# Kernel optimization log

Hardware: AMD Instinct MI355X
Metric: run time of the kernel (lower is better)

Reference implementation:

```python
import jax, jax.numpy as jnp
import numpy as np

EMB = 512
N_MODELS = 5
HID = 64
N_Q = 2048
N_P = 256


def setup_inputs() -> dict:
    key = jax.random.key(0)
    ks = jax.random.split(key, 6)
    return {
        "query_features": jax.random.normal(ks[0], (N_Q, EMB), dtype=jnp.float32),
        "prototypes": jax.random.normal(ks[1], (N_P, EMB), dtype=jnp.float32),
        # first Linear: weight [64, 2*EMB], bias [64], per model
        "W1": jax.random.normal(ks[2], (N_MODELS, HID, 2 * EMB), dtype=jnp.float32) * 0.02,
        "b1": jax.random.normal(ks[3], (N_MODELS, HID), dtype=jnp.float32) * 0.02,
        # second Linear: weight [1, 64] -> stored as [64], bias scalar per model
        "W2": jax.random.normal(ks[4], (N_MODELS, HID), dtype=jnp.float32) * 0.02,
        "b2": jax.random.normal(ks[5], (N_MODELS,), dtype=jnp.float32) * 0.02,
    }


def reference(query_features, prototypes, W1, b1, W2, b2):
    d = query_features.shape[1]
    # cat([q_i, p_j]) @ W1^T == q_i @ W1[:, :d]^T + p_j @ W1[:, d:]^T
    W1q = W1[:, :, :d]   # [M, H, d]
    W1p = W1[:, :, d:]   # [M, H, d]
    hq = jnp.einsum('qd,mhd->mqh', query_features, W1q)  # [M, Q, H]
    hp = jnp.einsum('pd,mhd->mph', prototypes, W1p)      # [M, P, H]
    h = jax.nn.relu(hq[:, :, None, :] + hp[:, None, :, :] + b1[:, None, None, :])  # [M, Q, P, H]
    out = jnp.einsum('mqph,mh->mqp', h, W2) + b2[:, None, None]  # [M, Q, P]
    mean_d = out.mean(axis=0)
    # torch.std default is unbiased (ddof=1)
    unc = jnp.std(out, axis=0, ddof=1)
    return mean_d * jnp.exp(-unc)
```

## Files before the change

kernel.cpp:

```cpp
#include <hip/hip_runtime.h>
#include <math.h>

#define EMB 512
#define NM 5
#define HID 64
#define NQ 2048
#define NP 256

typedef __attribute__((ext_vector_type(8))) short short8;
typedef __attribute__((ext_vector_type(4))) float floatx4;

#define A_BY 0u
#define B_BY 2621440u

#define LST 72

__device__ inline unsigned short bfr(float f) {
    unsigned u = __float_as_uint(f);
    u += 0x7FFFu + ((u >> 16) & 1u);
    return (unsigned short)(u >> 16);
}

__device__ inline void cvt8(float4 a, float4 b, short8& hi, short8& lo) {
#define C1(I, V) { unsigned short h_ = bfr(V); hi[I] = (short)h_; \
    lo[I] = (short)bfr(V - __uint_as_float(((unsigned)h_) << 16)); }
    C1(0, a.x) C1(1, a.y) C1(2, a.z) C1(3, a.w)
    C1(4, b.x) C1(5, b.y) C1(6, b.z) C1(7, b.w)
#undef C1
}
__device__ inline void cvt8hi(float4 a, float4 b, short8& hi) {
    hi[0] = (short)bfr(a.x); hi[1] = (short)bfr(a.y);
    hi[2] = (short)bfr(a.z); hi[3] = (short)bfr(a.w);
    hi[4] = (short)bfr(b.x); hi[5] = (short)bfr(b.y);
    hi[6] = (short)bfr(b.z); hi[7] = (short)bfr(b.w);
}

__global__ __launch_bounds__(256) void gemm_v3(const float* __restrict__ Q,
                                               const float* __restrict__ P,
                                               const float* __restrict__ W1,
                                               const float* __restrict__ b1,
                                               float* __restrict__ A,
                                               float* __restrict__ Bv) {
    __shared__ short XH[2][16 * LST];
    __shared__ short WH[2][64 * LST];
    __shared__ short WL[2][64 * LST];

    int tid  = threadIdx.x;
    int lane = tid & 63;
    int ht   = tid >> 6;
    int m    = blockIdx.x % 5;
    int rt   = blockIdx.x / 5;
    int r0   = rt * 16;
    bool isQ = rt < 128;

    int wrow = tid >> 3;
    int wg8  = (tid & 7) * 8;
    const float* wb  = W1 + (size_t)m * 64 * 1024 + (isQ ? 0 : EMB);
    const float* wp0 = wb + (size_t)wrow * 1024 + wg8;
    const float* wp1 = wb + (size_t)(wrow + 32) * 1024 + wg8;
    bool hasX = tid < 128;
    int xrow  = tid >> 3;
    const float* xp = (isQ ? Q + (size_t)(r0 + xrow) * EMB
                           : P + (size_t)(r0 - NQ + xrow) * EMB) + wg8;

    int arix = (lane & 15) * LST + (lane >> 4) * 8;
    int brix = (ht * 16 + (lane & 15)) * LST + (lane >> 4) * 8;

    floatx4 ac = {0, 0, 0, 0};
    float4 w00, w01, w10, w11, x0, x1;

    w00 = *(const float4*)&wp0[0]; w01 = *(const float4*)&wp0[4];
    w10 = *(const float4*)&wp1[0]; w11 = *(const float4*)&wp1[4];
    if (hasX) { x0 = *(const float4*)&xp[0]; x1 = *(const float4*)&xp[4]; }
    {
        short8 hi, lo;
        cvt8(w00, w01, hi, lo);
        *(short8*)&WH[0][wrow * LST + wg8] = hi;
        *(short8*)&WL[0][wrow * LST + wg8] = lo;
        cvt8(w10, w11, hi, lo);
        *(short8*)&WH[0][(wrow + 32) * LST + wg8] = hi;
        *(short8*)&WL[0][(wrow + 32) * LST + wg8] = lo;
        if (hasX) { short8 xh; cvt8hi(x0, x1, xh);
                    *(short8*)&XH[0][xrow * LST + wg8] = xh; }
    }

#pragma unroll 1
    for (int c = 0; c < 8; ++c) {
        int cur = c & 1;
        if (c < 7) {
            int k0 = (c + 1) * 64;
            w00 = *(const float4*)&wp0[k0]; w01 = *(const float4*)&wp0[k0 + 4];
            w10 = *(const float4*)&wp1[k0]; w11 = *(const float4*)&wp1[k0 + 4];
            if (hasX) { x0 = *(const float4*)&xp[k0]; x1 = *(const float4*)&xp[k0 + 4]; }
        }
        __syncthreads();

#pragma unroll
        for (int s = 0; s < 2; ++s) {
            short8 Ah = *(const short8*)&XH[cur][arix + s * 32];
            short8 Bh = *(const short8*)&WH[cur][brix + s * 32];
            short8 Bl = *(const short8*)&WL[cur][brix + s * 32];
            ac = __builtin_amdgcn_mfma_f32_16x16x32_bf16(Ah, Bl, ac, 0, 0, 0);
            ac = __builtin_amdgcn_mfma_f32_16x16x32_bf16(Ah, Bh, ac, 0, 0, 0);
        }

        if (c < 7) {
            int nb = cur ^ 1;
            short8 hi, lo;
            cvt8(w00, w01, hi, lo);
            *(short8*)&WH[nb][wrow * LST + wg8] = hi;
            *(short8*)&WL[nb][wrow * LST + wg8] = lo;
            cvt8(w10, w11, hi, lo);
            *(short8*)&WH[nb][(wrow + 32) * LST + wg8] = hi;
            *(short8*)&WL[nb][(wrow + 32) * LST + wg8] = lo;
            if (hasX) { short8 xh; cvt8hi(x0, x1, xh);
                        *(short8*)&XH[nb][xrow * LST + wg8] = xh; }
        }
    }

    int col  = lane & 15;
    int rloc = (lane >> 4) * 4;
    int hh   = ht * 16 + col;
    int rr   = r0 + rloc;

    if (isQ) {
        float bb = b1[m * 64 + hh];
        float* dst = &A[((size_t)m * NQ + rr) * HID + hh];
        dst[0 * HID] = ac.x + bb; dst[1 * HID] = ac.y + bb;
        dst[2 * HID] = ac.z + bb; dst[3 * HID] = ac.w + bb;
    } else {
        int p = rr - NQ;
        float* dst = &Bv[(((size_t)(m * 16 + (hh >> 2))) * NP + p) * 4 + (hh & 3)];
        dst[0 * 4] = ac.x; dst[1 * 4] = ac.y; dst[2 * 4] = ac.z; dst[3 * 4] = ac.w;
    }
}

__global__ __launch_bounds__(256) void fused_main(const float* __restrict__ A,
                                                  const float* __restrict__ Bv,
                                                  const float* __restrict__ W2,
                                                  const float* __restrict__ b2,
                                                  float* __restrict__ out) {
    int p  = threadIdx.x;
    int q0 = blockIdx.x * 2;

    float s1a = 0, s2a = 0, s1b = 0, s2b = 0;
    const float4* Bq = (const float4*)Bv + p;

#pragma unroll 1
    for (int m = 0; m < NM; ++m) {
        const float4* bm = Bq + (size_t)m * 16 * NP;
        float4 B0 = bm[0*NP],  B1 = bm[1*NP],  B2 = bm[2*NP],  B3 = bm[3*NP];
        float4 B4 = bm[4*NP],  B5 = bm[5*NP],  B6 = bm[6*NP],  B7 = bm[7*NP];
        float4 B8 = bm[8*NP],  B9 = bm[9*NP],  B10= bm[10*NP], B11= bm[11*NP];
        float4 B12= bm[12*NP], B13= bm[13*NP], B14= bm[14*NP], B15= bm[15*NP];

        const float* Ar  = A + ((size_t)m * NQ + q0) * HID;
        const float* Wp2 = W2 + m * HID;
        float oa = 0.f, ob = 0.f;

#define HSTEP(BF, H0) { \
        float wa=Wp2[H0+0], wb=Wp2[H0+1], wc=Wp2[H0+2], wd=Wp2[H0+3]; \
        oa = fmaf(fmaxf(Ar[H0+0]    + BF.x, 0.f), wa, oa); \
        oa = fmaf(fmaxf(Ar[H0+1]    + BF.y, 0.f), wb, oa); \
        oa = fmaf(fmaxf(Ar[H0+2]    + BF.z, 0.f), wc, oa); \
        oa = fmaf(fmaxf(Ar[H0+3]    + BF.w, 0.f), wd, oa); \
        ob = fmaf(fmaxf(Ar[64+H0+0] + BF.x, 0.f), wa, ob); \
        ob = fmaf(fmaxf(Ar[64+H0+1] + BF.y, 0.f), wb, ob); \
        ob = fmaf(fmaxf(Ar[64+H0+2] + BF.z, 0.f), wc, ob); \
        ob = fmaf(fmaxf(Ar[64+H0+3] + BF.w, 0.f), wd, ob); }

        HSTEP(B0,  0)  HSTEP(B1,  4)  HSTEP(B2,  8)  HSTEP(B3, 12)
        HSTEP(B4, 16)  HSTEP(B5, 20)  HSTEP(B6, 24)  HSTEP(B7, 28)
        HSTEP(B8, 32)  HSTEP(B9, 36)  HSTEP(B10,40)  HSTEP(B11,44)
        HSTEP(B12,48)  HSTEP(B13,52)  HSTEP(B14,56)  HSTEP(B15,60)
#undef HSTEP

        float bb = b2[m];
        float xa = oa + bb, xb = ob + bb;
        s1a += xa; s2a = fmaf(xa, xa, s2a);
        s1b += xb; s2b = fmaf(xb, xb, s2b);
    }

    {
        float mean = s1a * 0.2f;
        float var  = fmaxf((s2a - s1a * s1a * 0.2f) * 0.25f, 0.f);
        out[(size_t)q0 * NP + p] = mean * __expf(-sqrtf(var));
    }
    {
        float mean = s1b * 0.2f;
        float var  = fmaxf((s2b - s1b * s1b * 0.2f) * 0.25f, 0.f);
        out[(size_t)(q0 + 1) * NP + p] = mean * __expf(-sqrtf(var));
    }
}

extern "C" void kernel_launch(void* const* d_in, const int* in_sizes, int n_in,
                              void* d_out, int out_size, void* d_ws, size_t ws_size,
                              hipStream_t stream) {
    const float* Q  = (const float*)d_in[0];
    const float* P  = (const float*)d_in[1];
    const float* W1 = (const float*)d_in[2];
    const float* b1 = (const float*)d_in[3];
    const float* W2 = (const float*)d_in[4];
    const float* b2 = (const float*)d_in[5];
    float* out = (float*)d_out;

    char*  ws = (char*)d_ws;
    float* A  = (float*)(ws + A_BY);
    float* B  = (float*)(ws + B_BY);

    gemm_v3<<<720, 256, 0, stream>>>(Q, P, W1, b1, A, B);
    fused_main<<<1024, 256, 0, stream>>>(A, B, W2, b2, out);
}
```

Baseline: 93.83 us.

## Process 8 queries per block with prefetched B registers and packed float2 math

The fused main kernel now handles 8 queries per block instead of 2, so each thread reuses its per-prototype B values across four times as many queries and the grid shrinks from 1024 to 256 blocks. The next model's B vectors are loaded into a second register set while the current model is computed, and the hidden-dimension loop uses two-wide float vectors so the compiler can emit packed FP32 ops. The costs are much higher register pressure (two sets of 16 float4 plus 16 accumulators), which can lower occupancy, and a grid of only 256 blocks, roughly one block per compute unit, which leaves less room to hide latency.

```diff
diff --git a/kernel.cpp b/kernel.cpp
--- a/kernel.cpp
+++ b/kernel.cpp
@@ -9,6 +9,8 @@
 
 typedef __attribute__((ext_vector_type(8))) short short8;
 typedef __attribute__((ext_vector_type(4))) float floatx4;
+typedef __attribute__((ext_vector_type(4))) float vf4;
+typedef __attribute__((ext_vector_type(2))) float vf2;
 
 #define A_BY 0u
 #define B_BY 2621440u
@@ -141,55 +143,62 @@
                                                   const float* __restrict__ b2,
                                                   float* __restrict__ out) {
     int p  = threadIdx.x;
-    int q0 = blockIdx.x * 2;
-
-    float s1a = 0, s2a = 0, s1b = 0, s2b = 0;
-    const float4* Bq = (const float4*)Bv + p;
+    int q0 = blockIdx.x * 8;
+
+    const vf4* Bq = (const vf4*)Bv + p;
+
+    float s1[8], s2[8];
+#pragma unroll
+    for (int i = 0; i < 8; ++i) { s1[i] = 0.f; s2[i] = 0.f; }
+
+    vf4 Bc[16], Bn[16];
+#pragma unroll
+    for (int j = 0; j < 16; ++j) Bc[j] = Bq[j * NP];
 
 #pragma unroll 1
     for (int m = 0; m < NM; ++m) {
-        const float4* bm = Bq + (size_t)m * 16 * NP;
-        float4 B0 = bm[0*NP],  B1 = bm[1*NP],  B2 = bm[2*NP],  B3 = bm[3*NP];
-        float4 B4 = bm[4*NP],  B5 = bm[5*NP],  B6 = bm[6*NP],  B7 = bm[7*NP];
-        float4 B8 = bm[8*NP],  B9 = bm[9*NP],  B10= bm[10*NP], B11= bm[11*NP];
-        float4 B12= bm[12*NP], B13= bm[13*NP], B14= bm[14*NP], B15= bm[15*NP];
-
-        const float* Ar  = A + ((size_t)m * NQ + q0) * HID;
-        const float* Wp2 = W2 + m * HID;
-        float oa = 0.f, ob = 0.f;
-
-#define HSTEP(BF, H0) { \
-        float wa=Wp2[H0+0], wb=Wp2[H0+1], wc=Wp2[H0+2], wd=Wp2[H0+3]; \
-        oa = fmaf(fmaxf(Ar[H0+0]    + BF.x, 0.f), wa, oa); \
-        oa = fmaf(fmaxf(Ar[H0+1]    + BF.y, 0.f), wb, oa); \
-        oa = fmaf(fmaxf(Ar[H0+2]    + BF.z, 0.f), wc, oa); \
-        oa = fmaf(fmaxf(Ar[H0+3]    + BF.w, 0.f), wd, oa); \
-        ob = fmaf(fmaxf(Ar[64+H0+0] + BF.x, 0.f), wa, ob); \
-        ob = fmaf(fmaxf(Ar[64+H0+1] + BF.y, 0.f), wb, ob); \
-        ob = fmaf(fmaxf(Ar[64+H0+2] + BF.z, 0.f), wc, ob); \
-        ob = fmaf(fmaxf(Ar[64+H0+3] + BF.w, 0.f), wd, ob); }
-
-        HSTEP(B0,  0)  HSTEP(B1,  4)  HSTEP(B2,  8)  HSTEP(B3, 12)
-        HSTEP(B4, 16)  HSTEP(B5, 20)  HSTEP(B6, 24)  HSTEP(B7, 28)
-        HSTEP(B8, 32)  HSTEP(B9, 36)  HSTEP(B10,40)  HSTEP(B11,44)
-        HSTEP(B12,48)  HSTEP(B13,52)  HSTEP(B14,56)  HSTEP(B15,60)
-#undef HSTEP
-
+        if (m < NM - 1) {
+            const vf4* bn = Bq + (size_t)(m + 1) * 16 * NP;
+#pragma unroll
+            for (int j = 0; j < 16; ++j) Bn[j] = bn[j * NP];
+        }
+
+        const float* Am = A + ((size_t)m * NQ + q0) * HID;
+        const float* Wm = W2 + m * HID;
         float bb = b2[m];
-        float xa = oa + bb, xb = ob + bb;
-        s1a += xa; s2a = fmaf(xa, xa, s2a);
-        s1b += xb; s2b = fmaf(xb, xb, s2b);
-    }
-
-    {
-        float mean = s1a * 0.2f;
-        float var  = fmaxf((s2a - s1a * s1a * 0.2f) * 0.25f, 0.f);
-        out[(size_t)q0 * NP + p] = mean * __expf(-sqrtf(var));
-    }
-    {
-        float mean = s1b * 0.2f;
-        float var  = fmaxf((s2b - s1b * s1b * 0.2f) * 0.25f, 0.f);
-        out[(size_t)(q0 + 1) * NP + p] = mean * __expf(-sqrtf(var));
+
+#pragma unroll
+        for (int qi = 0; qi < 8; ++qi) {
+            const float* Ar = Am + qi * HID;
+            vf2 acc = {0.f, 0.f};
+#pragma unroll
+            for (int j = 0; j < 16; ++j) {
+                vf2 a0 = *(const vf2*)&Ar[j * 4 + 0];
+                vf2 a1 = *(const vf2*)&Ar[j * 4 + 2];
+                vf2 w0 = *(const vf2*)&Wm[j * 4 + 0];
+                vf2 w1 = *(const vf2*)&Wm[j * 4 + 2];
+                vf2 z  = {0.f, 0.f};
+                vf2 t0 = __builtin_elementwise_max(a0 + Bc[j].xy, z);
+                vf2 t1 = __builtin_elementwise_max(a1 + Bc[j].zw, z);
+                acc = t0 * w0 + acc;
+                acc = t1 * w1 + acc;
+            }
+            float x = acc.x + acc.y + bb;
+            s1[qi] += x;
+            s2[qi] = fmaf(x, x, s2[qi]);
+        }
+
+        if (m < NM - 1) {
+#pragma unroll
+            for (int j = 0; j < 16; ++j) Bc[j] = Bn[j];
+        }
+    }
+
+#pragma unroll
+    for (int qi = 0; qi < 8; ++qi) {
+        float mean = s1[qi] * 0.2f;
+        float var  = fmaxf((s2[qi] - s1[qi] * s1[qi] * 0.2f) * 0.25f, 0.f);
+        out[(size_t)(q0 + qi) * NP + p] = mean * __expf(-sqrtf(var));
     }
 }
 
@@ -209,5 +218,5 @@
     float* B  = (float*)(ws + B_BY);
 
     gemm_v3<<<720, 256, 0, stream>>>(Q, P, W1, b1, A, B);
-    fused_main<<<1024, 256, 0, stream>>>(A, B, W2, b2, out);
-}
+    fused_main<<<256, 256, 0, stream>>>(A, B, W2, b2, out);
+}
```

Result: slower. 141.1 us (+50.4%).
